# Optimization experiments

Hardware: AMD Instinct MI355X
Metric: run time of the kernel (lower is better)

## Reference

```python
import jax, jax.numpy as jnp
import numpy as np

N_NODES = 50000
N_EDGES = 800000
IN_FEATS, H_FEATS, N_CLASSES = 64, 64, 16


def setup_inputs() -> dict:
    key = jax.random.key(0)
    ks = jax.random.split(key, 8)
    x = jax.random.normal(ks[0], (N_NODES, IN_FEATS), dtype=jnp.float32)
    src = jax.random.randint(ks[1], (N_EDGES,), 0, N_NODES, dtype=jnp.int64)
    dst = jax.random.randint(ks[2], (N_EDGES,), 0, N_NODES, dtype=jnp.int64)
    W_self1 = jax.random.normal(ks[3], (IN_FEATS, H_FEATS), dtype=jnp.float32) / np.sqrt(IN_FEATS)
    W_neigh1 = jax.random.normal(ks[4], (IN_FEATS, H_FEATS), dtype=jnp.float32) / np.sqrt(IN_FEATS)
    b1 = jnp.zeros((H_FEATS,), dtype=jnp.float32)
    W_self2 = jax.random.normal(ks[5], (H_FEATS, N_CLASSES), dtype=jnp.float32) / np.sqrt(H_FEATS)
    W_neigh2 = jax.random.normal(ks[6], (H_FEATS, N_CLASSES), dtype=jnp.float32) / np.sqrt(H_FEATS)
    b2 = jnp.zeros((N_CLASSES,), dtype=jnp.float32)
    return {"x": x, "src": src, "dst": dst,
            "W_self1": W_self1, "W_neigh1": W_neigh1, "b1": b1,
            "W_self2": W_self2, "W_neigh2": W_neigh2, "b2": b2}


def _mean_agg(h, src, dst, n_nodes):
    # gather source-node features along edges, sum into destinations, divide by in-degree
    summed = jax.ops.segment_sum(h[src], dst, num_segments=n_nodes)  # [N, d]
    deg = jax.ops.segment_sum(jnp.ones_like(src, dtype=h.dtype), dst, num_segments=n_nodes)
    return summed / jnp.maximum(deg, 1.0)[:, None]  # zero in-degree -> zeros (DGL semantics)


def _sage_layer(h, src, dst, W_self, W_neigh, b):
    h_neigh = _mean_agg(h, src, dst, h.shape[0])
    return h @ W_self + h_neigh @ W_neigh + b


def reference(x, src, dst, W_self1, W_neigh1, b1, W_self2, W_neigh2, b2):
    h = _sage_layer(x, src, dst, W_self1, W_neigh1, b1)
    h = jax.nn.relu(h)
    out = _sage_layer(h, src, dst, W_self2, W_neigh2, b2)
    return out
```

## Files before the change

kernel.cpp:

```cpp
#include <hip/hip_runtime.h>
#include <hip/hip_bf16.h>
#include <cstring>


#define FEATS 64
#define CLS   16
#define EPT   16
#define CAP   5120
#define CAPN  64

typedef unsigned short bf16_t;
typedef float floatx2 __attribute__((ext_vector_type(2)));

__device__ __forceinline__ float bfbits2f(unsigned lo16) {
    unsigned v = lo16 << 16;
    float f;
    __builtin_memcpy(&f, &v, 4);
    return f;
}
__device__ __forceinline__ bf16_t f2bf(float f) {
    unsigned u;
    __builtin_memcpy(&u, &f, 4);
    u = (u + 0x7FFFu + ((u >> 16) & 1u)) >> 16;
    return (bf16_t)u;
}
__device__ __forceinline__ unsigned pack2(float a, float b) {
    return (unsigned)f2bf(a) | ((unsigned)f2bf(b) << 16);
}
__device__ __forceinline__ unsigned pack4_fp8(float a, float b, float c, float d) {
    int q = __builtin_amdgcn_cvt_pk_fp8_f32(a, b, 0, false);
    q = __builtin_amdgcn_cvt_pk_fp8_f32(c, d, q, true);
    return (unsigned)q;
}

__global__ __launch_bounds__(256) void fused_pg_kernel(
    const int* __restrict__ src, const int* __restrict__ dst,
    int* __restrict__ bucket_cnt, int* __restrict__ epart, int E,
    const float* __restrict__ x, const float* __restrict__ Ws,
    const float* __restrict__ Wn, bf16_t* __restrict__ selfo,
    unsigned char* __restrict__ t1, int N, int nbp)
{
    __shared__ float smem[16512];
    int t = threadIdx.x;

    if ((int)blockIdx.x < nbp) {
        int* hist = (int*)smem;
        int* base = hist + 256;
        int e0 = blockIdx.x * (256 * EPT);
        hist[t] = 0;
        __syncthreads();
        int pk[EPT];
        int bk[EPT];
#pragma unroll
        for (int j = 0; j < EPT; ++j) {
            int e = e0 + j * 256 + t;
            if (e < E) {
                int d = dst[e];
                pk[j] = (src[e] << 8) | (d & 255);
                bk[j] = d >> 8;
                atomicAdd(&hist[bk[j]], 1);
            } else bk[j] = -1;
        }
        __syncthreads();
        int c = hist[t];
        if (c) base[t] = atomicAdd(&bucket_cnt[t], c);
        hist[t] = 0;
        __syncthreads();
#pragma unroll
        for (int j = 0; j < EPT; ++j) {
            if (bk[j] >= 0) {
                int r = atomicAdd(&hist[bk[j]], 1);
                epart[bk[j] * CAP + base[bk[j]] + r] = pk[j];
            }
        }
        return;
    }

    float* Wc = smem;
    float* xs = smem + 8192;
    int node0 = ((int)blockIdx.x - nbp) * 128;

    for (int idx = t; idx < 64 * 128; idx += 256) {
        int k = idx >> 7, c = idx & 127;
        Wc[idx] = (c < 64) ? Ws[k * 64 + c] : Wn[k * 64 + (c - 64)];
    }
    for (int idx = t; idx < 128 * 16; idx += 256) {
        int row = idx >> 4, c4 = idx & 15;
        int node = node0 + row;
        float4 v = (node < N) ? ((const float4*)(x + (size_t)node * 64))[c4]
                              : make_float4(0.f, 0.f, 0.f, 0.f);
        float* p = &xs[row * 65 + c4 * 4];
        p[0] = v.x; p[1] = v.y; p[2] = v.z; p[3] = v.w;
    }
    __syncthreads();

    int m = t & 31;
    int g = t >> 5;
    float acc[4][16];
#pragma unroll
    for (int j = 0; j < 4; ++j)
#pragma unroll
        for (int c = 0; c < 16; ++c) acc[j][c] = 0.f;

    for (int k = 0; k < 64; ++k) {
        float w[16];
        const float* wp = &Wc[k * 128 + g * 16];
#pragma unroll
        for (int c = 0; c < 16; ++c) w[c] = wp[c];
        float a0 = xs[m * 65 + k];
        float a1 = xs[(m + 32) * 65 + k];
        float a2 = xs[(m + 64) * 65 + k];
        float a3 = xs[(m + 96) * 65 + k];
#pragma unroll
        for (int c = 0; c < 16; ++c) {
            acc[0][c] += a0 * w[c];
            acc[1][c] += a1 * w[c];
            acc[2][c] += a2 * w[c];
            acc[3][c] += a3 * w[c];
        }
    }
#pragma unroll
    for (int j = 0; j < 4; ++j) {
        int node = node0 + m + 32 * j;
        if (node < N) {
            if (g < 4) {
                bf16_t* dstp = selfo + (size_t)node * 64 + g * 16;
                uint4 p0, p1;
                p0.x = pack2(acc[j][0],  acc[j][1]);  p0.y = pack2(acc[j][2],  acc[j][3]);
                p0.z = pack2(acc[j][4],  acc[j][5]);  p0.w = pack2(acc[j][6],  acc[j][7]);
                p1.x = pack2(acc[j][8],  acc[j][9]);  p1.y = pack2(acc[j][10], acc[j][11]);
                p1.z = pack2(acc[j][12], acc[j][13]); p1.w = pack2(acc[j][14], acc[j][15]);
                *(uint4*)(dstp) = p0;
                *(uint4*)(dstp + 8) = p1;
            } else {
                unsigned char* dstp = t1 + (size_t)node * 64 + (g - 4) * 16;
                uint4 q;
                q.x = pack4_fp8(acc[j][0],  acc[j][1],  acc[j][2],  acc[j][3]);
                q.y = pack4_fp8(acc[j][4],  acc[j][5],  acc[j][6],  acc[j][7]);
                q.z = pack4_fp8(acc[j][8],  acc[j][9],  acc[j][10], acc[j][11]);
                q.w = pack4_fp8(acc[j][12], acc[j][13], acc[j][14], acc[j][15]);
                *(uint4*)(dstp) = q;
            }
        }
    }
}

__global__ __launch_bounds__(256) void buildcsr_kernel(const int* __restrict__ epart,
                                                       const int* __restrict__ bucket_cnt,
                                                       int* __restrict__ cnt,
                                                       int* __restrict__ csr, int N) {
    __shared__ int c[256];
    int t = threadIdx.x;
    int b = blockIdx.x;
    int ebeg = b * CAP;
    int ecnt = bucket_cnt[b];
    c[t] = 0;
    __syncthreads();
    for (int e = t; e < ecnt; e += 256) {
        int pk = epart[ebeg + e];
        int ln = pk & 255;
        int r = atomicAdd(&c[ln], 1);
        if (r < CAPN) csr[(size_t)(b * 256 + ln) * CAPN + r] = pk >> 8;
    }
    __syncthreads();
    int node = b * 256 + t;
    if (node < N) cnt[node] = c[t];
}

__global__ __launch_bounds__(256) void gather64_kernel(
    const int* __restrict__ csr, const int* __restrict__ cnt,
    const unsigned char* __restrict__ t1, const bf16_t* __restrict__ selfo,
    bf16_t* __restrict__ h1, const float* __restrict__ b1, int N)
{
    int wid = (blockIdx.x * 256 + threadIdx.x) >> 6;
    int lane = threadIdx.x & 63;
    int eslot = lane >> 4;
    int cg = lane & 15;
    if (wid >= N) return;
    int eraw = csr[(size_t)wid * CAPN + lane];
    int d = cnt[wid];
    size_t o = (size_t)wid * 64 + cg * 4;
    uint2 su;
    float4 bb;
    if (eslot == 0) {
        su = *(const uint2*)(selfo + o);
        bb = *(const float4*)(b1 + cg * 4);
    }
    d = min(d, CAPN);
    float ax = 0.f, ay = 0.f, az = 0.f, aw = 0.f;
    if (d > 0) {
        int dm1 = d - 1;
#define G64_ACC(r, m)                                                      \
        {                                                                  \
            floatx2 p_ = __builtin_amdgcn_cvt_pk_f32_fp8((int)(r), false); \
            floatx2 q_ = __builtin_amdgcn_cvt_pk_f32_fp8((int)(r), true);  \
            ax += (m) * p_.x; ay += (m) * p_.y;                            \
            az += (m) * q_.x; aw += (m) * q_.y;                            \
        }
#define G64_BATCH(KN)                                                      \
        {                                                                  \
            int ss[KN];                                                    \
            float mk[KN];                                                  \
            unsigned rr[KN];                                               \
            _Pragma("unroll")                                              \
            for (int k = 0; k < KN; ++k) {                                 \
                int i = eslot + 4 * k;                                     \
                int idx = i > dm1 ? dm1 : i;                               \
                mk[k] = (i <= dm1) ? 1.f : 0.f;                            \
                ss[k] = __shfl(eraw, idx);                                 \
            }                                                              \
            _Pragma("unroll")                                              \
            for (int k = 0; k < KN; ++k)                                   \
                rr[k] = *(const unsigned*)(t1 + (size_t)ss[k] * 64 + cg * 4); \
            _Pragma("unroll")                                              \
            for (int k = 0; k < KN; ++k) G64_ACC(rr[k], mk[k]);            \
        }
        if (d <= 16) {
            G64_BATCH(4)
        } else if (d <= 32) {
            G64_BATCH(8)
        } else {
            G64_BATCH(16)
        }
#undef G64_BATCH
#undef G64_ACC
        ax += __shfl_xor(ax, 16); ay += __shfl_xor(ay, 16);
        az += __shfl_xor(az, 16); aw += __shfl_xor(aw, 16);
        ax += __shfl_xor(ax, 32); ay += __shfl_xor(ay, 32);
        az += __shfl_xor(az, 32); aw += __shfl_xor(aw, 32);
    }
    if (eslot == 0) {
        float inv = 1.f / fmaxf((float)d, 1.f);
        float rx = fmaxf(bfbits2f(su.x & 0xffff) + ax * inv + bb.x, 0.f);
        float ry = fmaxf(bfbits2f(su.x >> 16)    + ay * inv + bb.y, 0.f);
        float rz = fmaxf(bfbits2f(su.y & 0xffff) + az * inv + bb.z, 0.f);
        float rw = fmaxf(bfbits2f(su.y >> 16)    + aw * inv + bb.w, 0.f);
        uint2 pk;
        pk.x = pack2(rx, ry);
        pk.y = pack2(rz, rw);
        *(uint2*)(h1 + o) = pk;
    }
}

__global__ __launch_bounds__(256) void gather16_kernel(
    const int* __restrict__ csr, const int* __restrict__ cnt,
    const bf16_t* __restrict__ t2,
    float* __restrict__ outp, const float* __restrict__ b2, int N)
{
    int wid = (blockIdx.x * 256 + threadIdx.x) >> 6;
    int lane = threadIdx.x & 63;
    int eslot = lane >> 3;
    int c2 = lane & 7;
    if (wid >= N) return;
    int eraw = csr[(size_t)wid * CAPN + lane];
    int d = cnt[wid];
    size_t o = (size_t)wid * 16 + c2 * 2;
    float2 oo = make_float2(0.f, 0.f), bbv = make_float2(0.f, 0.f);
    if (eslot == 0) {
        oo = *(const float2*)(outp + o);
        bbv = *(const float2*)(b2 + c2 * 2);
    }
    d = min(d, CAPN);
    float a0 = 0.f, a1 = 0.f;
    if (d > 0) {
        int dm1 = d - 1;
#define G16_BATCH(KN)                                                      \
        {                                                                  \
            int ss[KN];                                                    \
            float mk[KN];                                                  \
            unsigned uu[KN];                                               \
            _Pragma("unroll")                                              \
            for (int k = 0; k < KN; ++k) {                                 \
                int i = eslot + 8 * k;                                     \
                int idx = i > dm1 ? dm1 : i;                               \
                mk[k] = (i <= dm1) ? 1.f : 0.f;                            \
                ss[k] = __shfl(eraw, idx);                                 \
            }                                                              \
            _Pragma("unroll")                                              \
            for (int k = 0; k < KN; ++k)                                   \
                uu[k] = *(const unsigned*)(t2 + (size_t)ss[k] * 16 + c2 * 2); \
            _Pragma("unroll")                                              \
            for (int k = 0; k < KN; ++k) {                                 \
                a0 += mk[k] * bfbits2f(uu[k] & 0xffff);                    \
                a1 += mk[k] * bfbits2f(uu[k] >> 16);                       \
            }                                                              \
        }
        if (d <= 16) {
            G16_BATCH(2)
        } else if (d <= 32) {
            G16_BATCH(4)
        } else {
            G16_BATCH(8)
        }
#undef G16_BATCH
        a0 += __shfl_xor(a0, 8);  a1 += __shfl_xor(a1, 8);
        a0 += __shfl_xor(a0, 16); a1 += __shfl_xor(a1, 16);
        a0 += __shfl_xor(a0, 32); a1 += __shfl_xor(a1, 32);
    }
    if (eslot == 0) {
        float inv = 1.f / fmaxf((float)d, 1.f);
        float2 r;
        r.x = oo.x + a0 * inv + bbv.x;
        r.y = oo.y + a1 * inv + bbv.y;
        *(float2*)(outp + o) = r;
    }
}

__global__ __launch_bounds__(256) void gemm2_kernel(
    const bf16_t* __restrict__ h1, const float* __restrict__ Ws,
    const float* __restrict__ Wn, float* __restrict__ outp,
    bf16_t* __restrict__ t2, int N)
{
    __shared__ float Wc[64 * 32];
    __shared__ float xs[128 * 65];
    int t = threadIdx.x;
    int node0 = blockIdx.x * 128;

    for (int idx = t; idx < 64 * 32; idx += 256) {
        int k = idx >> 5, c = idx & 31;
        Wc[idx] = (c < 16) ? Ws[k * 16 + c] : Wn[k * 16 + (c - 16)];
    }
    for (int idx = t; idx < 128 * 8; idx += 256) {
        int row = idx >> 3, c8 = idx & 7;
        int node = node0 + row;
        float* p = &xs[row * 65 + c8 * 8];
        if (node < N) {
            uint4 u = *(const uint4*)(h1 + (size_t)node * 64 + c8 * 8);
            p[0] = bfbits2f(u.x & 0xffff); p[1] = bfbits2f(u.x >> 16);
            p[2] = bfbits2f(u.y & 0xffff); p[3] = bfbits2f(u.y >> 16);
            p[4] = bfbits2f(u.z & 0xffff); p[5] = bfbits2f(u.z >> 16);
            p[6] = bfbits2f(u.w & 0xffff); p[7] = bfbits2f(u.w >> 16);
        } else {
            for (int qq = 0; qq < 8; ++qq) p[qq] = 0.f;
        }
    }
    __syncthreads();

    int m = t & 31;
    int g = t >> 5;
    float acc[4][4];
#pragma unroll
    for (int j = 0; j < 4; ++j)
#pragma unroll
        for (int c = 0; c < 4; ++c) acc[j][c] = 0.f;

    for (int k = 0; k < 64; ++k) {
        float w[4];
        const float* wp = &Wc[k * 32 + g * 4];
#pragma unroll
        for (int c = 0; c < 4; ++c) w[c] = wp[c];
        float a0 = xs[m * 65 + k];
        float a1 = xs[(m + 32) * 65 + k];
        float a2 = xs[(m + 64) * 65 + k];
        float a3 = xs[(m + 96) * 65 + k];
#pragma unroll
        for (int c = 0; c < 4; ++c) {
            acc[0][c] += a0 * w[c];
            acc[1][c] += a1 * w[c];
            acc[2][c] += a2 * w[c];
            acc[3][c] += a3 * w[c];
        }
    }
#pragma unroll
    for (int j = 0; j < 4; ++j) {
        int node = node0 + m + 32 * j;
        if (node < N) {
            if (g < 4) {
                *(float4*)(outp + (size_t)node * 16 + g * 4) =
                    make_float4(acc[j][0], acc[j][1], acc[j][2], acc[j][3]);
            } else {
                uint2 pk;
                pk.x = pack2(acc[j][0], acc[j][1]);
                pk.y = pack2(acc[j][2], acc[j][3]);
                *(uint2*)(t2 + (size_t)node * 16 + (g - 4) * 4) = pk;
            }
        }
    }
}

extern "C" void kernel_launch(void* const* d_in, const int* in_sizes, int n_in,
                              void* d_out, int out_size, void* d_ws, size_t ws_size,
                              hipStream_t stream) {
    const float* x   = (const float*)d_in[0];
    const int*   src = (const int*)d_in[1];
    const int*   dst = (const int*)d_in[2];
    const float* Ws1 = (const float*)d_in[3];
    const float* Wn1 = (const float*)d_in[4];
    const float* b1  = (const float*)d_in[5];
    const float* Ws2 = (const float*)d_in[6];
    const float* Wn2 = (const float*)d_in[7];
    const float* b2  = (const float*)d_in[8];
    float* outp = (float*)d_out;

    const int N = in_sizes[0] / FEATS;
    const int E = in_sizes[1];
    const int B = (N + 255) / 256;
    const int NBP = (E + 256 * EPT - 1) / (256 * EPT);
    const int NBG = (N + 127) / 128;

    char* p = (char*)d_ws;
    auto align16 = [](char* q) { return (char*)(((size_t)q + 15) & ~(size_t)15); };
    int* bucket_cnt    = (int*)p;                  p = (char*)(bucket_cnt + 256);
    int* epart         = (int*)p;                  p = (char*)(epart + (size_t)B * CAP);
    int* cnt           = (int*)align16(p);         p = (char*)(cnt + N);
    int* csr           = (int*)align16(p);         p = (char*)(csr + (size_t)N * CAPN);
    bf16_t* selfo      = (bf16_t*)align16(p);      p = (char*)(selfo + (size_t)N * 64);
    unsigned char* t1  = (unsigned char*)align16(p); p = (char*)(t1 + (size_t)N * 64);
    bf16_t* h1         = (bf16_t*)align16(p);      p = (char*)(h1 + (size_t)N * 64);
    bf16_t* t2         = (bf16_t*)align16(p);

    hipMemsetAsync(bucket_cnt, 0, 256 * sizeof(int), stream);

    fused_pg_kernel<<<NBP + NBG, 256, 0, stream>>>(
        src, dst, bucket_cnt, epart, E, x, Ws1, Wn1, selfo, t1, N, NBP);
    buildcsr_kernel<<<B, 256, 0, stream>>>(epart, bucket_cnt, cnt, csr, N);

    gather64_kernel<<<((size_t)N * 64 + 255) / 256, 256, 0, stream>>>(
        csr, cnt, t1, selfo, h1, b1, N);
    gemm2_kernel<<<(N + 127) / 128, 256, 0, stream>>>(h1, Ws2, Wn2, outp, t2, N);
    gather16_kernel<<<((size_t)N * 64 + 255) / 256, 256, 0, stream>>>(
        csr, cnt, t2, outp, b2, N);
}
```

Before: 152.5 us.

## Merge all stages into one persistent cooperative kernel with grid syncs

Replaces the five separate launches (partition+GEMM1, CSR build, gather64, GEMM2, gather16) with one persistent cooperative kernel. The stages run as grid-stride loops separated by grid.sync(), which removes per-launch overhead and the idle gaps between kernels. GEMM tiles shrink from 128 to 64 nodes so the smaller shared-memory footprint allows three blocks per CU. In exchange, each stage is limited to a fixed grid, grid-wide barriers add cost, and register pressure under launch bounds of 3 may cause spills.

```diff
diff --git a/kernel.cpp b/kernel.cpp
--- a/kernel.cpp
+++ b/kernel.cpp
@@ -1,6 +1,9 @@
 #include <hip/hip_runtime.h>
+#include <hip/hip_cooperative_groups.h>
 #include <hip/hip_bf16.h>
 #include <cstring>
+
+namespace cgr = cooperative_groups;
 
 
 #define FEATS 64
@@ -8,6 +11,7 @@
 #define EPT   16
 #define CAP   5120
 #define CAPN  64
+#define SMEMF 12352
 
 typedef unsigned short bf16_t;
 typedef float floatx2 __attribute__((ext_vector_type(2)));
@@ -33,346 +37,330 @@
     return (unsigned)q;
 }
 
-__global__ __launch_bounds__(256) void fused_pg_kernel(
+__global__ __launch_bounds__(256, 3) void mega_kernel(
     const int* __restrict__ src, const int* __restrict__ dst,
-    int* __restrict__ bucket_cnt, int* __restrict__ epart, int E,
-    const float* __restrict__ x, const float* __restrict__ Ws,
-    const float* __restrict__ Wn, bf16_t* __restrict__ selfo,
-    unsigned char* __restrict__ t1, int N, int nbp)
+    int* __restrict__ bucket_cnt, int* __restrict__ epart,
+    int* __restrict__ cnt, int* __restrict__ csr,
+    const float* __restrict__ x,
+    const float* __restrict__ Ws1, const float* __restrict__ Wn1,
+    const float* __restrict__ b1,
+    const float* __restrict__ Ws2, const float* __restrict__ Wn2,
+    const float* __restrict__ b2,
+    bf16_t* __restrict__ selfo, unsigned char* __restrict__ t1,
+    bf16_t* __restrict__ h1, bf16_t* __restrict__ t2,
+    float* __restrict__ outp, int N, int E)
 {
-    __shared__ float smem[16512];
-    int t = threadIdx.x;
-
-    if ((int)blockIdx.x < nbp) {
-        int* hist = (int*)smem;
-        int* base = hist + 256;
-        int e0 = blockIdx.x * (256 * EPT);
-        hist[t] = 0;
+    __shared__ float smem[SMEMF];
+    cgr::grid_group grid = cgr::this_grid();
+    const int t = threadIdx.x;
+    const int nb = gridDim.x;
+    const int NP = (E + 256 * EPT - 1) / (256 * EPT);
+    const int NT = (N + 63) / 64;
+    const int B  = (N + 255) / 256;
+
+    for (int u = (int)blockIdx.x; u < NP + NT; u += nb) {
+        if (u < NP) {
+            int* hist = (int*)smem;
+            int* base = hist + 256;
+            int e0 = u * (256 * EPT);
+            hist[t] = 0;
+            __syncthreads();
+            int pk[EPT], bk[EPT];
+#pragma unroll
+            for (int j = 0; j < EPT; ++j) {
+                int e = e0 + j * 256 + t;
+                if (e < E) {
+                    int d = dst[e];
+                    pk[j] = (src[e] << 8) | (d & 255);
+                    bk[j] = d >> 8;
+                    atomicAdd(&hist[bk[j]], 1);
+                } else bk[j] = -1;
+            }
+            __syncthreads();
+            int c0 = hist[t];
+            if (c0) base[t] = atomicAdd(&bucket_cnt[t], c0);
+            hist[t] = 0;
+            __syncthreads();
+#pragma unroll
+            for (int j = 0; j < EPT; ++j) {
+                if (bk[j] >= 0) {
+                    int r = atomicAdd(&hist[bk[j]], 1);
+                    epart[bk[j] * CAP + base[bk[j]] + r] = pk[j];
+                }
+            }
+            __syncthreads();
+        } else {
+            int node0 = (u - NP) * 64;
+            float* Wc = smem;
+            float* xs = smem + 8192;
+            for (int idx = t; idx < 64 * 128; idx += 256) {
+                int k = idx >> 7, c = idx & 127;
+                Wc[idx] = (c < 64) ? Ws1[k * 64 + c] : Wn1[k * 64 + (c - 64)];
+            }
+            for (int idx = t; idx < 64 * 16; idx += 256) {
+                int row = idx >> 4, c4 = idx & 15;
+                int node = node0 + row;
+                float4 v = (node < N) ? ((const float4*)(x + (size_t)node * 64))[c4]
+                                      : make_float4(0.f, 0.f, 0.f, 0.f);
+                float* pp = &xs[row * 65 + c4 * 4];
+                pp[0] = v.x; pp[1] = v.y; pp[2] = v.z; pp[3] = v.w;
+            }
+            __syncthreads();
+            int m = t & 31;
+            int g = t >> 5;
+            float acc[2][16];
+#pragma unroll
+            for (int j = 0; j < 2; ++j)
+#pragma unroll
+                for (int c = 0; c < 16; ++c) acc[j][c] = 0.f;
+            for (int k = 0; k < 64; ++k) {
+                float w[16];
+                const float* wp = &Wc[k * 128 + g * 16];
+#pragma unroll
+                for (int c = 0; c < 16; ++c) w[c] = wp[c];
+                float a0 = xs[m * 65 + k];
+                float a1 = xs[(m + 32) * 65 + k];
+#pragma unroll
+                for (int c = 0; c < 16; ++c) {
+                    acc[0][c] += a0 * w[c];
+                    acc[1][c] += a1 * w[c];
+                }
+            }
+#pragma unroll
+            for (int j = 0; j < 2; ++j) {
+                int node = node0 + m + 32 * j;
+                if (node < N) {
+                    if (g < 4) {
+                        bf16_t* dstp = selfo + (size_t)node * 64 + g * 16;
+                        uint4 p0, p1;
+                        p0.x = pack2(acc[j][0],  acc[j][1]);  p0.y = pack2(acc[j][2],  acc[j][3]);
+                        p0.z = pack2(acc[j][4],  acc[j][5]);  p0.w = pack2(acc[j][6],  acc[j][7]);
+                        p1.x = pack2(acc[j][8],  acc[j][9]);  p1.y = pack2(acc[j][10], acc[j][11]);
+                        p1.z = pack2(acc[j][12], acc[j][13]); p1.w = pack2(acc[j][14], acc[j][15]);
+                        *(uint4*)(dstp) = p0;
+                        *(uint4*)(dstp + 8) = p1;
+                    } else {
+                        unsigned char* dstp = t1 + (size_t)node * 64 + (g - 4) * 16;
+                        uint4 q;
+                        q.x = pack4_fp8(acc[j][0],  acc[j][1],  acc[j][2],  acc[j][3]);
+                        q.y = pack4_fp8(acc[j][4],  acc[j][5],  acc[j][6],  acc[j][7]);
+                        q.z = pack4_fp8(acc[j][8],  acc[j][9],  acc[j][10], acc[j][11]);
+                        q.w = pack4_fp8(acc[j][12], acc[j][13], acc[j][14], acc[j][15]);
+                        *(uint4*)(dstp) = q;
+                    }
+                }
+            }
+            __syncthreads();
+        }
+    }
+    grid.sync();
+
+    for (int u = (int)blockIdx.x; u < B; u += nb) {
+        int* c = (int*)smem;
+        int ebeg = u * CAP;
+        int ecnt = bucket_cnt[u];
+        c[t] = 0;
         __syncthreads();
-        int pk[EPT];
-        int bk[EPT];
-#pragma unroll
-        for (int j = 0; j < EPT; ++j) {
-            int e = e0 + j * 256 + t;
-            if (e < E) {
-                int d = dst[e];
-                pk[j] = (src[e] << 8) | (d & 255);
-                bk[j] = d >> 8;
-                atomicAdd(&hist[bk[j]], 1);
-            } else bk[j] = -1;
+        for (int e = t; e < ecnt; e += 256) {
+            int pk = epart[ebeg + e];
+            int ln = pk & 255;
+            int r = atomicAdd(&c[ln], 1);
+            if (r < CAPN) csr[(size_t)(u * 256 + ln) * CAPN + r] = pk >> 8;
         }
         __syncthreads();
-        int c = hist[t];
-        if (c) base[t] = atomicAdd(&bucket_cnt[t], c);
-        hist[t] = 0;
+        int node = u * 256 + t;
+        if (node < N) cnt[node] = c[t];
         __syncthreads();
-#pragma unroll
-        for (int j = 0; j < EPT; ++j) {
-            if (bk[j] >= 0) {
-                int r = atomicAdd(&hist[bk[j]], 1);
-                epart[bk[j] * CAP + base[bk[j]] + r] = pk[j];
-            }
-        }
-        return;
-    }
-
-    float* Wc = smem;
-    float* xs = smem + 8192;
-    int node0 = ((int)blockIdx.x - nbp) * 128;
-
-    for (int idx = t; idx < 64 * 128; idx += 256) {
-        int k = idx >> 7, c = idx & 127;
-        Wc[idx] = (c < 64) ? Ws[k * 64 + c] : Wn[k * 64 + (c - 64)];
-    }
-    for (int idx = t; idx < 128 * 16; idx += 256) {
-        int row = idx >> 4, c4 = idx & 15;
-        int node = node0 + row;
-        float4 v = (node < N) ? ((const float4*)(x + (size_t)node * 64))[c4]
-                              : make_float4(0.f, 0.f, 0.f, 0.f);
-        float* p = &xs[row * 65 + c4 * 4];
-        p[0] = v.x; p[1] = v.y; p[2] = v.z; p[3] = v.w;
-    }
-    __syncthreads();
-
-    int m = t & 31;
-    int g = t >> 5;
-    float acc[4][16];
-#pragma unroll
-    for (int j = 0; j < 4; ++j)
-#pragma unroll
-        for (int c = 0; c < 16; ++c) acc[j][c] = 0.f;
-
-    for (int k = 0; k < 64; ++k) {
-        float w[16];
-        const float* wp = &Wc[k * 128 + g * 16];
-#pragma unroll
-        for (int c = 0; c < 16; ++c) w[c] = wp[c];
-        float a0 = xs[m * 65 + k];
-        float a1 = xs[(m + 32) * 65 + k];
-        float a2 = xs[(m + 64) * 65 + k];
-        float a3 = xs[(m + 96) * 65 + k];
-#pragma unroll
-        for (int c = 0; c < 16; ++c) {
-            acc[0][c] += a0 * w[c];
-            acc[1][c] += a1 * w[c];
-            acc[2][c] += a2 * w[c];
-            acc[3][c] += a3 * w[c];
-        }
-    }
-#pragma unroll
-    for (int j = 0; j < 4; ++j) {
-        int node = node0 + m + 32 * j;
-        if (node < N) {
-            if (g < 4) {
-                bf16_t* dstp = selfo + (size_t)node * 64 + g * 16;
-                uint4 p0, p1;
-                p0.x = pack2(acc[j][0],  acc[j][1]);  p0.y = pack2(acc[j][2],  acc[j][3]);
-                p0.z = pack2(acc[j][4],  acc[j][5]);  p0.w = pack2(acc[j][6],  acc[j][7]);
-                p1.x = pack2(acc[j][8],  acc[j][9]);  p1.y = pack2(acc[j][10], acc[j][11]);
-                p1.z = pack2(acc[j][12], acc[j][13]); p1.w = pack2(acc[j][14], acc[j][15]);
-                *(uint4*)(dstp) = p0;
-                *(uint4*)(dstp + 8) = p1;
-            } else {
-                unsigned char* dstp = t1 + (size_t)node * 64 + (g - 4) * 16;
-                uint4 q;
-                q.x = pack4_fp8(acc[j][0],  acc[j][1],  acc[j][2],  acc[j][3]);
-                q.y = pack4_fp8(acc[j][4],  acc[j][5],  acc[j][6],  acc[j][7]);
-                q.z = pack4_fp8(acc[j][8],  acc[j][9],  acc[j][10], acc[j][11]);
-                q.w = pack4_fp8(acc[j][12], acc[j][13], acc[j][14], acc[j][15]);
-                *(uint4*)(dstp) = q;
-            }
-        }
-    }
-}
-
-__global__ __launch_bounds__(256) void buildcsr_kernel(const int* __restrict__ epart,
-                                                       const int* __restrict__ bucket_cnt,
-                                                       int* __restrict__ cnt,
-                                                       int* __restrict__ csr, int N) {
-    __shared__ int c[256];
-    int t = threadIdx.x;
-    int b = blockIdx.x;
-    int ebeg = b * CAP;
-    int ecnt = bucket_cnt[b];
-    c[t] = 0;
-    __syncthreads();
-    for (int e = t; e < ecnt; e += 256) {
-        int pk = epart[ebeg + e];
-        int ln = pk & 255;
-        int r = atomicAdd(&c[ln], 1);
-        if (r < CAPN) csr[(size_t)(b * 256 + ln) * CAPN + r] = pk >> 8;
-    }
-    __syncthreads();
-    int node = b * 256 + t;
-    if (node < N) cnt[node] = c[t];
-}
-
-__global__ __launch_bounds__(256) void gather64_kernel(
-    const int* __restrict__ csr, const int* __restrict__ cnt,
-    const unsigned char* __restrict__ t1, const bf16_t* __restrict__ selfo,
-    bf16_t* __restrict__ h1, const float* __restrict__ b1, int N)
-{
-    int wid = (blockIdx.x * 256 + threadIdx.x) >> 6;
-    int lane = threadIdx.x & 63;
-    int eslot = lane >> 4;
-    int cg = lane & 15;
-    if (wid >= N) return;
-    int eraw = csr[(size_t)wid * CAPN + lane];
-    int d = cnt[wid];
-    size_t o = (size_t)wid * 64 + cg * 4;
-    uint2 su;
-    float4 bb;
-    if (eslot == 0) {
-        su = *(const uint2*)(selfo + o);
-        bb = *(const float4*)(b1 + cg * 4);
-    }
-    d = min(d, CAPN);
-    float ax = 0.f, ay = 0.f, az = 0.f, aw = 0.f;
-    if (d > 0) {
-        int dm1 = d - 1;
+    }
+    grid.sync();
+
+    {
+        const int lane = t & 63;
+        const int eslot = lane >> 4;
+        const int cg4 = lane & 15;
+        const int gw = (int)blockIdx.x * 4 + (t >> 6);
+        for (int wid = gw; wid < N; wid += nb * 4) {
+            int eraw = csr[(size_t)wid * CAPN + lane];
+            int d = cnt[wid];
+            size_t o = (size_t)wid * 64 + cg4 * 4;
+            uint2 su; float4 bb;
+            if (eslot == 0) {
+                su = *(const uint2*)(selfo + o);
+                bb = *(const float4*)(b1 + cg4 * 4);
+            }
+            d = min(d, CAPN);
+            float ax = 0.f, ay = 0.f, az = 0.f, aw = 0.f;
+            if (d > 0) {
+                int dm1 = d - 1;
 #define G64_ACC(r, m)                                                      \
-        {                                                                  \
-            floatx2 p_ = __builtin_amdgcn_cvt_pk_f32_fp8((int)(r), false); \
-            floatx2 q_ = __builtin_amdgcn_cvt_pk_f32_fp8((int)(r), true);  \
-            ax += (m) * p_.x; ay += (m) * p_.y;                            \
-            az += (m) * q_.x; aw += (m) * q_.y;                            \
-        }
+                {                                                          \
+                    floatx2 p_ = __builtin_amdgcn_cvt_pk_f32_fp8((int)(r), false); \
+                    floatx2 q_ = __builtin_amdgcn_cvt_pk_f32_fp8((int)(r), true);  \
+                    ax += (m) * p_.x; ay += (m) * p_.y;                    \
+                    az += (m) * q_.x; aw += (m) * q_.y;                    \
+                }
 #define G64_BATCH(KN)                                                      \
-        {                                                                  \
-            int ss[KN];                                                    \
-            float mk[KN];                                                  \
-            unsigned rr[KN];                                               \
-            _Pragma("unroll")                                              \
-            for (int k = 0; k < KN; ++k) {                                 \
-                int i = eslot + 4 * k;                                     \
-                int idx = i > dm1 ? dm1 : i;                               \
-                mk[k] = (i <= dm1) ? 1.f : 0.f;                            \
-                ss[k] = __shfl(eraw, idx);                                 \
-            }                                                              \
-            _Pragma("unroll")                                              \
-            for (int k = 0; k < KN; ++k)                                   \
-                rr[k] = *(const unsigned*)(t1 + (size_t)ss[k] * 64 + cg * 4); \
-            _Pragma("unroll")                                              \
-            for (int k = 0; k < KN; ++k) G64_ACC(rr[k], mk[k]);            \
-        }
-        if (d <= 16) {
-            G64_BATCH(4)
-        } else if (d <= 32) {
-            G64_BATCH(8)
-        } else {
-            G64_BATCH(16)
-        }
+                {                                                          \
+                    int ss[KN]; float mk[KN]; unsigned rr[KN];             \
+                    _Pragma("unroll")                                      \
+                    for (int k = 0; k < KN; ++k) {                         \
+                        int i = eslot + 4 * k;                             \
+                        int idx = i > dm1 ? dm1 : i;                       \
+                        mk[k] = (i <= dm1) ? 1.f : 0.f;                    \
+                        ss[k] = __shfl(eraw, idx);                         \
+                    }                                                      \
+                    _Pragma("unroll")                                      \
+                    for (int k = 0; k < KN; ++k)                           \
+                        rr[k] = *(const unsigned*)(t1 + (size_t)ss[k] * 64 + cg4 * 4); \
+                    _Pragma("unroll")                                      \
+                    for (int k = 0; k < KN; ++k) G64_ACC(rr[k], mk[k]);    \
+                }
+                if (d <= 16) {
+                    G64_BATCH(4)
+                } else if (d <= 32) {
+                    G64_BATCH(8)
+                } else {
+                    G64_BATCH(16)
+                }
 #undef G64_BATCH
 #undef G64_ACC
-        ax += __shfl_xor(ax, 16); ay += __shfl_xor(ay, 16);
-        az += __shfl_xor(az, 16); aw += __shfl_xor(aw, 16);
-        ax += __shfl_xor(ax, 32); ay += __shfl_xor(ay, 32);
-        az += __shfl_xor(az, 32); aw += __shfl_xor(aw, 32);
-    }
-    if (eslot == 0) {
-        float inv = 1.f / fmaxf((float)d, 1.f);
-        float rx = fmaxf(bfbits2f(su.x & 0xffff) + ax * inv + bb.x, 0.f);
-        float ry = fmaxf(bfbits2f(su.x >> 16)    + ay * inv + bb.y, 0.f);
-        float rz = fmaxf(bfbits2f(su.y & 0xffff) + az * inv + bb.z, 0.f);
-        float rw = fmaxf(bfbits2f(su.y >> 16)    + aw * inv + bb.w, 0.f);
-        uint2 pk;
-        pk.x = pack2(rx, ry);
-        pk.y = pack2(rz, rw);
-        *(uint2*)(h1 + o) = pk;
-    }
-}
-
-__global__ __launch_bounds__(256) void gather16_kernel(
-    const int* __restrict__ csr, const int* __restrict__ cnt,
-    const bf16_t* __restrict__ t2,
-    float* __restrict__ outp, const float* __restrict__ b2, int N)
-{
-    int wid = (blockIdx.x * 256 + threadIdx.x) >> 6;
-    int lane = threadIdx.x & 63;
-    int eslot = lane >> 3;
-    int c2 = lane & 7;
-    if (wid >= N) return;
-    int eraw = csr[(size_t)wid * CAPN + lane];
-    int d = cnt[wid];
-    size_t o = (size_t)wid * 16 + c2 * 2;
-    float2 oo = make_float2(0.f, 0.f), bbv = make_float2(0.f, 0.f);
-    if (eslot == 0) {
-        oo = *(const float2*)(outp + o);
-        bbv = *(const float2*)(b2 + c2 * 2);
-    }
-    d = min(d, CAPN);
-    float a0 = 0.f, a1 = 0.f;
-    if (d > 0) {
-        int dm1 = d - 1;
+                ax += __shfl_xor(ax, 16); ay += __shfl_xor(ay, 16);
+                az += __shfl_xor(az, 16); aw += __shfl_xor(aw, 16);
+                ax += __shfl_xor(ax, 32); ay += __shfl_xor(ay, 32);
+                az += __shfl_xor(az, 32); aw += __shfl_xor(aw, 32);
+            }
+            if (eslot == 0) {
+                float inv = 1.f / fmaxf((float)d, 1.f);
+                float rx = fmaxf(bfbits2f(su.x & 0xffff) + ax * inv + bb.x, 0.f);
+                float ry = fmaxf(bfbits2f(su.x >> 16)    + ay * inv + bb.y, 0.f);
+                float rz = fmaxf(bfbits2f(su.y & 0xffff) + az * inv + bb.z, 0.f);
+                float rw = fmaxf(bfbits2f(su.y >> 16)    + aw * inv + bb.w, 0.f);
+                uint2 pk;
+                pk.x = pack2(rx, ry);
+                pk.y = pack2(rz, rw);
+                *(uint2*)(h1 + o) = pk;
+            }
+        }
+    }
+    grid.sync();
+
+    for (int u = (int)blockIdx.x; u < NT; u += nb) {
+        int node0 = u * 64;
+        float* Wc2 = smem;
+        float* xs2 = smem + 2048;
+        for (int idx = t; idx < 64 * 32; idx += 256) {
+            int k = idx >> 5, c = idx & 31;
+            Wc2[idx] = (c < 16) ? Ws2[k * 16 + c] : Wn2[k * 16 + (c - 16)];
+        }
+        for (int idx = t; idx < 64 * 8; idx += 256) {
+            int row = idx >> 3, c8 = idx & 7;
+            int node = node0 + row;
+            float* pp = &xs2[row * 65 + c8 * 8];
+            if (node < N) {
+                uint4 uv = *(const uint4*)(h1 + (size_t)node * 64 + c8 * 8);
+                pp[0] = bfbits2f(uv.x & 0xffff); pp[1] = bfbits2f(uv.x >> 16);
+                pp[2] = bfbits2f(uv.y & 0xffff); pp[3] = bfbits2f(uv.y >> 16);
+                pp[4] = bfbits2f(uv.z & 0xffff); pp[5] = bfbits2f(uv.z >> 16);
+                pp[6] = bfbits2f(uv.w & 0xffff); pp[7] = bfbits2f(uv.w >> 16);
+            } else {
+                for (int qq = 0; qq < 8; ++qq) pp[qq] = 0.f;
+            }
+        }
+        __syncthreads();
+        int m = t & 31;
+        int g = t >> 5;
+        float acc[2][4];
+#pragma unroll
+        for (int j = 0; j < 2; ++j)
+#pragma unroll
+            for (int c = 0; c < 4; ++c) acc[j][c] = 0.f;
+        for (int k = 0; k < 64; ++k) {
+            float w[4];
+            const float* wp = &Wc2[k * 32 + g * 4];
+#pragma unroll
+            for (int c = 0; c < 4; ++c) w[c] = wp[c];
+            float a0 = xs2[m * 65 + k];
+            float a1 = xs2[(m + 32) * 65 + k];
+#pragma unroll
+            for (int c = 0; c < 4; ++c) {
+                acc[0][c] += a0 * w[c];
+                acc[1][c] += a1 * w[c];
+            }
+        }
+#pragma unroll
+        for (int j = 0; j < 2; ++j) {
+            int node = node0 + m + 32 * j;
+            if (node < N) {
+                if (g < 4) {
+                    *(float4*)(outp + (size_t)node * 16 + g * 4) =
+                        make_float4(acc[j][0], acc[j][1], acc[j][2], acc[j][3]);
+                } else {
+                    uint2 pk;
+                    pk.x = pack2(acc[j][0], acc[j][1]);
+                    pk.y = pack2(acc[j][2], acc[j][3]);
+                    *(uint2*)(t2 + (size_t)node * 16 + (g - 4) * 4) = pk;
+                }
+            }
+        }
+        __syncthreads();
+    }
+    grid.sync();
+
+    {
+        const int lane = t & 63;
+        const int eslot = lane >> 3;
+        const int c2 = lane & 7;
+        const int gw = (int)blockIdx.x * 4 + (t >> 6);
+        for (int wid = gw; wid < N; wid += nb * 4) {
+            int eraw = csr[(size_t)wid * CAPN + lane];
+            int d = cnt[wid];
+            size_t o = (size_t)wid * 16 + c2 * 2;
+            float2 oo = make_float2(0.f, 0.f), bbv = make_float2(0.f, 0.f);
+            if (eslot == 0) {
+                oo = *(const float2*)(outp + o);
+                bbv = *(const float2*)(b2 + c2 * 2);
+            }
+            d = min(d, CAPN);
+            float a0 = 0.f, a1 = 0.f;
+            if (d > 0) {
+                int dm1 = d - 1;
 #define G16_BATCH(KN)                                                      \
-        {                                                                  \
-            int ss[KN];                                                    \
-            float mk[KN];                                                  \
-            unsigned uu[KN];                                               \
-            _Pragma("unroll")                                              \
-            for (int k = 0; k < KN; ++k) {                                 \
-                int i = eslot + 8 * k;                                     \
-                int idx = i > dm1 ? dm1 : i;                               \
-                mk[k] = (i <= dm1) ? 1.f : 0.f;                            \
-                ss[k] = __shfl(eraw, idx);                                 \
-            }                                                              \
-            _Pragma("unroll")                                              \
-            for (int k = 0; k < KN; ++k)                                   \
-                uu[k] = *(const unsigned*)(t2 + (size_t)ss[k] * 16 + c2 * 2); \
-            _Pragma("unroll")                                              \
-            for (int k = 0; k < KN; ++k) {                                 \
-                a0 += mk[k] * bfbits2f(uu[k] & 0xffff);                    \
-                a1 += mk[k] * bfbits2f(uu[k] >> 16);                       \
-            }                                                              \
-        }
-        if (d <= 16) {
-            G16_BATCH(2)
-        } else if (d <= 32) {
-            G16_BATCH(4)
-        } else {
-            G16_BATCH(8)
-        }
+                {                                                          \
+                    int ss[KN]; float mk[KN]; unsigned uu[KN];             \
+                    _Pragma("unroll")                                      \
+                    for (int k = 0; k < KN; ++k) {                         \
+                        int i = eslot + 8 * k;                             \
+                        int idx = i > dm1 ? dm1 : i;                       \
+                        mk[k] = (i <= dm1) ? 1.f : 0.f;                    \
+                        ss[k] = __shfl(eraw, idx);                         \
+                    }                                                      \
+                    _Pragma("unroll")                                      \
+                    for (int k = 0; k < KN; ++k)                           \
+                        uu[k] = *(const unsigned*)(t2 + (size_t)ss[k] * 16 + c2 * 2); \
+                    _Pragma("unroll")                                      \
+                    for (int k = 0; k < KN; ++k) {                         \
+                        a0 += mk[k] * bfbits2f(uu[k] & 0xffff);            \
+                        a1 += mk[k] * bfbits2f(uu[k] >> 16);               \
+                    }                                                      \
+                }
+                if (d <= 16) {
+                    G16_BATCH(2)
+                } else if (d <= 32) {
+                    G16_BATCH(4)
+                } else {
+                    G16_BATCH(8)
+                }
 #undef G16_BATCH
-        a0 += __shfl_xor(a0, 8);  a1 += __shfl_xor(a1, 8);
-        a0 += __shfl_xor(a0, 16); a1 += __shfl_xor(a1, 16);
-        a0 += __shfl_xor(a0, 32); a1 += __shfl_xor(a1, 32);
-    }
-    if (eslot == 0) {
-        float inv = 1.f / fmaxf((float)d, 1.f);
-        float2 r;
-        r.x = oo.x + a0 * inv + bbv.x;
-        r.y = oo.y + a1 * inv + bbv.y;
-        *(float2*)(outp + o) = r;
-    }
-}
-
-__global__ __launch_bounds__(256) void gemm2_kernel(
-    const bf16_t* __restrict__ h1, const float* __restrict__ Ws,
-    const float* __restrict__ Wn, float* __restrict__ outp,
-    bf16_t* __restrict__ t2, int N)
-{
-    __shared__ float Wc[64 * 32];
-    __shared__ float xs[128 * 65];
-    int t = threadIdx.x;
-    int node0 = blockIdx.x * 128;
-
-    for (int idx = t; idx < 64 * 32; idx += 256) {
-        int k = idx >> 5, c = idx & 31;
-        Wc[idx] = (c < 16) ? Ws[k * 16 + c] : Wn[k * 16 + (c - 16)];
-    }
-    for (int idx = t; idx < 128 * 8; idx += 256) {
-        int row = idx >> 3, c8 = idx & 7;
-        int node = node0 + row;
-        float* p = &xs[row * 65 + c8 * 8];
-        if (node < N) {
-            uint4 u = *(const uint4*)(h1 + (size_t)node * 64 + c8 * 8);
-            p[0] = bfbits2f(u.x & 0xffff); p[1] = bfbits2f(u.x >> 16);
-            p[2] = bfbits2f(u.y & 0xffff); p[3] = bfbits2f(u.y >> 16);
-            p[4] = bfbits2f(u.z & 0xffff); p[5] = bfbits2f(u.z >> 16);
-            p[6] = bfbits2f(u.w & 0xffff); p[7] = bfbits2f(u.w >> 16);
-        } else {
-            for (int qq = 0; qq < 8; ++qq) p[qq] = 0.f;
-        }
-    }
-    __syncthreads();
-
-    int m = t & 31;
-    int g = t >> 5;
-    float acc[4][4];
-#pragma unroll
-    for (int j = 0; j < 4; ++j)
-#pragma unroll
-        for (int c = 0; c < 4; ++c) acc[j][c] = 0.f;
-
-    for (int k = 0; k < 64; ++k) {
-        float w[4];
-        const float* wp = &Wc[k * 32 + g * 4];
-#pragma unroll
-        for (int c = 0; c < 4; ++c) w[c] = wp[c];
-        float a0 = xs[m * 65 + k];
-        float a1 = xs[(m + 32) * 65 + k];
-        float a2 = xs[(m + 64) * 65 + k];
-        float a3 = xs[(m + 96) * 65 + k];
-#pragma unroll
-        for (int c = 0; c < 4; ++c) {
-            acc[0][c] += a0 * w[c];
-            acc[1][c] += a1 * w[c];
-            acc[2][c] += a2 * w[c];
-            acc[3][c] += a3 * w[c];
-        }
-    }
-#pragma unroll
-    for (int j = 0; j < 4; ++j) {
-        int node = node0 + m + 32 * j;
-        if (node < N) {
-            if (g < 4) {
-                *(float4*)(outp + (size_t)node * 16 + g * 4) =
-                    make_float4(acc[j][0], acc[j][1], acc[j][2], acc[j][3]);
-            } else {
-                uint2 pk;
-                pk.x = pack2(acc[j][0], acc[j][1]);
-                pk.y = pack2(acc[j][2], acc[j][3]);
-                *(uint2*)(t2 + (size_t)node * 16 + (g - 4) * 4) = pk;
+                a0 += __shfl_xor(a0, 8);  a1 += __shfl_xor(a1, 8);
+                a0 += __shfl_xor(a0, 16); a1 += __shfl_xor(a1, 16);
+                a0 += __shfl_xor(a0, 32); a1 += __shfl_xor(a1, 32);
+            }
+            if (eslot == 0) {
+                float inv = 1.f / fmaxf((float)d, 1.f);
+                float2 r;
+                r.x = oo.x + a0 * inv + bbv.x;
+                r.y = oo.y + a1 * inv + bbv.y;
+                *(float2*)(outp + o) = r;
             }
         }
     }
@@ -381,9 +369,9 @@
 extern "C" void kernel_launch(void* const* d_in, const int* in_sizes, int n_in,
                               void* d_out, int out_size, void* d_ws, size_t ws_size,
                               hipStream_t stream) {
+    const int* srcp = (const int*)d_in[1];
+    const int* dstp = (const int*)d_in[2];
     const float* x   = (const float*)d_in[0];
-    const int*   src = (const int*)d_in[1];
-    const int*   dst = (const int*)d_in[2];
     const float* Ws1 = (const float*)d_in[3];
     const float* Wn1 = (const float*)d_in[4];
     const float* b1  = (const float*)d_in[5];
@@ -392,11 +380,9 @@
     const float* b2  = (const float*)d_in[8];
     float* outp = (float*)d_out;
 
-    const int N = in_sizes[0] / FEATS;
-    const int E = in_sizes[1];
+    int N = in_sizes[0] / FEATS;
+    int E = in_sizes[1];
     const int B = (N + 255) / 256;
-    const int NBP = (E + 256 * EPT - 1) / (256 * EPT);
-    const int NBG = (N + 127) / 128;
 
     char* p = (char*)d_ws;
     auto align16 = [](char* q) { return (char*)(((size_t)q + 15) & ~(size_t)15); };
@@ -409,15 +395,29 @@
     bf16_t* h1         = (bf16_t*)align16(p);      p = (char*)(h1 + (size_t)N * 64);
     bf16_t* t2         = (bf16_t*)align16(p);
 
+    static int grid_blocks = 0;
+    if (grid_blocks == 0) {
+        int bpc = 0;
+        if (hipOccupancyMaxActiveBlocksPerMultiprocessor(&bpc, mega_kernel, 256, 0)
+                != hipSuccess || bpc <= 0)
+            bpc = 2;
+        int ncu = 256;
+        hipDeviceProp_t prop;
+        if (hipGetDeviceProperties(&prop, 0) == hipSuccess && prop.multiProcessorCount > 0)
+            ncu = prop.multiProcessorCount;
+        grid_blocks = bpc * ncu;
+    }
+
     hipMemsetAsync(bucket_cnt, 0, 256 * sizeof(int), stream);
 
-    fused_pg_kernel<<<NBP + NBG, 256, 0, stream>>>(
-        src, dst, bucket_cnt, epart, E, x, Ws1, Wn1, selfo, t1, N, NBP);
-    buildcsr_kernel<<<B, 256, 0, stream>>>(epart, bucket_cnt, cnt, csr, N);
-
-    gather64_kernel<<<((size_t)N * 64 + 255) / 256, 256, 0, stream>>>(
-        csr, cnt, t1, selfo, h1, b1, N);
-    gemm2_kernel<<<(N + 127) / 128, 256, 0, stream>>>(h1, Ws2, Wn2, outp, t2, N);
-    gather16_kernel<<<((size_t)N * 64 + 255) / 256, 256, 0, stream>>>(
-        csr, cnt, t2, outp, b2, N);
-}
+    void* kargs[] = {
+        (void*)&srcp, (void*)&dstp, (void*)&bucket_cnt, (void*)&epart,
+        (void*)&cnt, (void*)&csr, (void*)&x,
+        (void*)&Ws1, (void*)&Wn1, (void*)&b1,
+        (void*)&Ws2, (void*)&Wn2, (void*)&b2,
+        (void*)&selfo, (void*)&t1, (void*)&h1, (void*)&t2,
+        (void*)&outp, (void*)&N, (void*)&E
+    };
+    hipLaunchCooperativeKernel((void*)mega_kernel, dim3(grid_blocks), dim3(256),
+                               kargs, 0, stream);
+}
```

New measurement: 483.7 us. 217% more time.

## Fuse layer-1 neighbor gather with layer-2 GEMM via shared memory

Applied to the files above, without the earlier changes.

Merges the 64-wide gather kernel and the second-layer GEMM into one kernel. Each block of 256 threads gathers 64 nodes (16 rows per wave) into a shared fp32 tile, then runs the 64x32 projection to produce the self output and t2. This removes the h1 bf16 round trip through global memory and one kernel launch. In exchange, each block now processes its gather rows sequentially and uses more shared memory, which could lower occupancy and latency hiding for the irregular gather loads.

```diff
diff --git a/kernel.cpp b/kernel.cpp
--- a/kernel.cpp
+++ b/kernel.cpp
@@ -167,78 +167,129 @@
     if (node < N) cnt[node] = c[t];
 }
 
-__global__ __launch_bounds__(256) void gather64_kernel(
+__global__ __launch_bounds__(256) void fused_g64g2_kernel(
     const int* __restrict__ csr, const int* __restrict__ cnt,
     const unsigned char* __restrict__ t1, const bf16_t* __restrict__ selfo,
-    bf16_t* __restrict__ h1, const float* __restrict__ b1, int N)
+    const float* __restrict__ b1,
+    const float* __restrict__ Ws2, const float* __restrict__ Wn2,
+    float* __restrict__ outp, bf16_t* __restrict__ t2, int N)
 {
-    int wid = (blockIdx.x * 256 + threadIdx.x) >> 6;
-    int lane = threadIdx.x & 63;
+    __shared__ float Wc[64 * 32];
+    __shared__ float xs[64 * 65];
+    int t = threadIdx.x;
+    int node0 = blockIdx.x * 64;
+
+    for (int idx = t; idx < 64 * 32; idx += 256) {
+        int k = idx >> 5, c = idx & 31;
+        Wc[idx] = (c < 16) ? Ws2[k * 16 + c] : Wn2[k * 16 + (c - 16)];
+    }
+
+    int wv = t >> 6;
+    int lane = t & 63;
     int eslot = lane >> 4;
-    int cg = lane & 15;
-    if (wid >= N) return;
-    int eraw = csr[(size_t)wid * CAPN + lane];
-    int d = cnt[wid];
-    size_t o = (size_t)wid * 64 + cg * 4;
-    uint2 su;
-    float4 bb;
-    if (eslot == 0) {
-        su = *(const uint2*)(selfo + o);
-        bb = *(const float4*)(b1 + cg * 4);
-    }
-    d = min(d, CAPN);
-    float ax = 0.f, ay = 0.f, az = 0.f, aw = 0.f;
-    if (d > 0) {
-        int dm1 = d - 1;
+    int cg4 = lane & 15;
+    float4 bb = *(const float4*)(b1 + cg4 * 4);
+
+    for (int it = 0; it < 16; ++it) {
+        int row = it * 4 + wv;
+        int wid = node0 + row;
+        if (wid < N) {
+            int eraw = csr[(size_t)wid * CAPN + lane];
+            int d = cnt[wid];
+            size_t o = (size_t)wid * 64 + cg4 * 4;
+            uint2 su;
+            if (eslot == 0) su = *(const uint2*)(selfo + o);
+            d = min(d, CAPN);
+            float ax = 0.f, ay = 0.f, az = 0.f, aw = 0.f;
+            if (d > 0) {
+                int dm1 = d - 1;
 #define G64_ACC(r, m)                                                      \
-        {                                                                  \
-            floatx2 p_ = __builtin_amdgcn_cvt_pk_f32_fp8((int)(r), false); \
-            floatx2 q_ = __builtin_amdgcn_cvt_pk_f32_fp8((int)(r), true);  \
-            ax += (m) * p_.x; ay += (m) * p_.y;                            \
-            az += (m) * q_.x; aw += (m) * q_.y;                            \
-        }
+                {                                                          \
+                    floatx2 p_ = __builtin_amdgcn_cvt_pk_f32_fp8((int)(r), false); \
+                    floatx2 q_ = __builtin_amdgcn_cvt_pk_f32_fp8((int)(r), true);  \
+                    ax += (m) * p_.x; ay += (m) * p_.y;                    \
+                    az += (m) * q_.x; aw += (m) * q_.y;                    \
+                }
 #define G64_BATCH(KN)                                                      \
-        {                                                                  \
-            int ss[KN];                                                    \
-            float mk[KN];                                                  \
-            unsigned rr[KN];                                               \
-            _Pragma("unroll")                                              \
-            for (int k = 0; k < KN; ++k) {                                 \
-                int i = eslot + 4 * k;                                     \
-                int idx = i > dm1 ? dm1 : i;                               \
-                mk[k] = (i <= dm1) ? 1.f : 0.f;                            \
-                ss[k] = __shfl(eraw, idx);                                 \
-            }                                                              \
-            _Pragma("unroll")                                              \
-            for (int k = 0; k < KN; ++k)                                   \
-                rr[k] = *(const unsigned*)(t1 + (size_t)ss[k] * 64 + cg * 4); \
-            _Pragma("unroll")                                              \
-            for (int k = 0; k < KN; ++k) G64_ACC(rr[k], mk[k]);            \
-        }
-        if (d <= 16) {
-            G64_BATCH(4)
-        } else if (d <= 32) {
-            G64_BATCH(8)
-        } else {
-            G64_BATCH(16)
-        }
+                {                                                          \
+                    int ss[KN]; float mk[KN]; unsigned rr[KN];             \
+                    _Pragma("unroll")                                      \
+                    for (int k = 0; k < KN; ++k) {                         \
+                        int i = eslot + 4 * k;                             \
+                        int idx = i > dm1 ? dm1 : i;                       \
+                        mk[k] = (i <= dm1) ? 1.f : 0.f;                    \
+                        ss[k] = __shfl(eraw, idx);                         \
+                    }                                                      \
+                    _Pragma("unroll")                                      \
+                    for (int k = 0; k < KN; ++k)                           \
+                        rr[k] = *(const unsigned*)(t1 + (size_t)ss[k] * 64 + cg4 * 4); \
+                    _Pragma("unroll")                                      \
+                    for (int k = 0; k < KN; ++k) G64_ACC(rr[k], mk[k]);    \
+                }
+                if (d <= 16) {
+                    G64_BATCH(4)
+                } else if (d <= 32) {
+                    G64_BATCH(8)
+                } else {
+                    G64_BATCH(16)
+                }
 #undef G64_BATCH
 #undef G64_ACC
-        ax += __shfl_xor(ax, 16); ay += __shfl_xor(ay, 16);
-        az += __shfl_xor(az, 16); aw += __shfl_xor(aw, 16);
-        ax += __shfl_xor(ax, 32); ay += __shfl_xor(ay, 32);
-        az += __shfl_xor(az, 32); aw += __shfl_xor(aw, 32);
-    }
-    if (eslot == 0) {
-        float inv = 1.f / fmaxf((float)d, 1.f);
-        float rx = fmaxf(bfbits2f(su.x & 0xffff) + ax * inv + bb.x, 0.f);
-        float ry = fmaxf(bfbits2f(su.x >> 16)    + ay * inv + bb.y, 0.f);
-        float rz = fmaxf(bfbits2f(su.y & 0xffff) + az * inv + bb.z, 0.f);
-        float rw = fmaxf(bfbits2f(su.y >> 16)    + aw * inv + bb.w, 0.f);
-        uint2 pk;
-        pk.x = pack2(rx, ry);
-        pk.y = pack2(rz, rw);
-        *(uint2*)(h1 + o) = pk;
+                ax += __shfl_xor(ax, 16); ay += __shfl_xor(ay, 16);
+                az += __shfl_xor(az, 16); aw += __shfl_xor(aw, 16);
+                ax += __shfl_xor(ax, 32); ay += __shfl_xor(ay, 32);
+                az += __shfl_xor(az, 32); aw += __shfl_xor(aw, 32);
+            }
+            if (eslot == 0) {
+                float inv = 1.f / fmaxf((float)d, 1.f);
+                float* pp = &xs[row * 65 + cg4 * 4];
+                pp[0] = fmaxf(bfbits2f(su.x & 0xffff) + ax * inv + bb.x, 0.f);
+                pp[1] = fmaxf(bfbits2f(su.x >> 16)    + ay * inv + bb.y, 0.f);
+                pp[2] = fmaxf(bfbits2f(su.y & 0xffff) + az * inv + bb.z, 0.f);
+                pp[3] = fmaxf(bfbits2f(su.y >> 16)    + aw * inv + bb.w, 0.f);
+            }
+        } else if (eslot == 0) {
+            float* pp = &xs[row * 65 + cg4 * 4];
+            pp[0] = 0.f; pp[1] = 0.f; pp[2] = 0.f; pp[3] = 0.f;
+        }
+    }
+    __syncthreads();
+
+    int m = t & 31;
+    int g = t >> 5;
+    float acc[2][4];
+#pragma unroll
+    for (int j = 0; j < 2; ++j)
+#pragma unroll
+        for (int c = 0; c < 4; ++c) acc[j][c] = 0.f;
+
+    for (int k = 0; k < 64; ++k) {
+        float w[4];
+        const float* wp = &Wc[k * 32 + g * 4];
+#pragma unroll
+        for (int c = 0; c < 4; ++c) w[c] = wp[c];
+        float a0 = xs[m * 65 + k];
+        float a1 = xs[(m + 32) * 65 + k];
+#pragma unroll
+        for (int c = 0; c < 4; ++c) {
+            acc[0][c] += a0 * w[c];
+            acc[1][c] += a1 * w[c];
+        }
+    }
+#pragma unroll
+    for (int j = 0; j < 2; ++j) {
+        int node = node0 + m + 32 * j;
+        if (node < N) {
+            if (g < 4) {
+                *(float4*)(outp + (size_t)node * 16 + g * 4) =
+                    make_float4(acc[j][0], acc[j][1], acc[j][2], acc[j][3]);
+            } else {
+                uint2 pk;
+                pk.x = pack2(acc[j][0], acc[j][1]);
+                pk.y = pack2(acc[j][2], acc[j][3]);
+                *(uint2*)(t2 + (size_t)node * 16 + (g - 4) * 4) = pk;
+            }
+        }
     }
 }
 
@@ -266,9 +317,7 @@
         int dm1 = d - 1;
 #define G16_BATCH(KN)                                                      \
         {                                                                  \
-            int ss[KN];                                                    \
-            float mk[KN];                                                  \
-            unsigned uu[KN];                                               \
+            int ss[KN]; float mk[KN]; unsigned uu[KN];                     \
             _Pragma("unroll")                                              \
             for (int k = 0; k < KN; ++k) {                                 \
                 int i = eslot + 8 * k;                                     \
@@ -306,78 +355,6 @@
     }
 }
 
-__global__ __launch_bounds__(256) void gemm2_kernel(
-    const bf16_t* __restrict__ h1, const float* __restrict__ Ws,
-    const float* __restrict__ Wn, float* __restrict__ outp,
-    bf16_t* __restrict__ t2, int N)
-{
-    __shared__ float Wc[64 * 32];
-    __shared__ float xs[128 * 65];
-    int t = threadIdx.x;
-    int node0 = blockIdx.x * 128;
-
-    for (int idx = t; idx < 64 * 32; idx += 256) {
-        int k = idx >> 5, c = idx & 31;
-        Wc[idx] = (c < 16) ? Ws[k * 16 + c] : Wn[k * 16 + (c - 16)];
-    }
-    for (int idx = t; idx < 128 * 8; idx += 256) {
-        int row = idx >> 3, c8 = idx & 7;
-        int node = node0 + row;
-        float* p = &xs[row * 65 + c8 * 8];
-        if (node < N) {
-            uint4 u = *(const uint4*)(h1 + (size_t)node * 64 + c8 * 8);
-            p[0] = bfbits2f(u.x & 0xffff); p[1] = bfbits2f(u.x >> 16);
-            p[2] = bfbits2f(u.y & 0xffff); p[3] = bfbits2f(u.y >> 16);
-            p[4] = bfbits2f(u.z & 0xffff); p[5] = bfbits2f(u.z >> 16);
-            p[6] = bfbits2f(u.w & 0xffff); p[7] = bfbits2f(u.w >> 16);
-        } else {
-            for (int qq = 0; qq < 8; ++qq) p[qq] = 0.f;
-        }
-    }
-    __syncthreads();
-
-    int m = t & 31;
-    int g = t >> 5;
-    float acc[4][4];
-#pragma unroll
-    for (int j = 0; j < 4; ++j)
-#pragma unroll
-        for (int c = 0; c < 4; ++c) acc[j][c] = 0.f;
-
-    for (int k = 0; k < 64; ++k) {
-        float w[4];
-        const float* wp = &Wc[k * 32 + g * 4];
-#pragma unroll
-        for (int c = 0; c < 4; ++c) w[c] = wp[c];
-        float a0 = xs[m * 65 + k];
-        float a1 = xs[(m + 32) * 65 + k];
-        float a2 = xs[(m + 64) * 65 + k];
-        float a3 = xs[(m + 96) * 65 + k];
-#pragma unroll
-        for (int c = 0; c < 4; ++c) {
-            acc[0][c] += a0 * w[c];
-            acc[1][c] += a1 * w[c];
-            acc[2][c] += a2 * w[c];
-            acc[3][c] += a3 * w[c];
-        }
-    }
-#pragma unroll
-    for (int j = 0; j < 4; ++j) {
-        int node = node0 + m + 32 * j;
-        if (node < N) {
-            if (g < 4) {
-                *(float4*)(outp + (size_t)node * 16 + g * 4) =
-                    make_float4(acc[j][0], acc[j][1], acc[j][2], acc[j][3]);
-            } else {
-                uint2 pk;
-                pk.x = pack2(acc[j][0], acc[j][1]);
-                pk.y = pack2(acc[j][2], acc[j][3]);
-                *(uint2*)(t2 + (size_t)node * 16 + (g - 4) * 4) = pk;
-            }
-        }
-    }
-}
-
 extern "C" void kernel_launch(void* const* d_in, const int* in_sizes, int n_in,
                               void* d_out, int out_size, void* d_ws, size_t ws_size,
                               hipStream_t stream) {
@@ -397,6 +374,7 @@
     const int B = (N + 255) / 256;
     const int NBP = (E + 256 * EPT - 1) / (256 * EPT);
     const int NBG = (N + 127) / 128;
+    const int NG2 = (N + 63) / 64;
 
     char* p = (char*)d_ws;
     auto align16 = [](char* q) { return (char*)(((size_t)q + 15) & ~(size_t)15); };
@@ -406,7 +384,6 @@
     int* csr           = (int*)align16(p);         p = (char*)(csr + (size_t)N * CAPN);
     bf16_t* selfo      = (bf16_t*)align16(p);      p = (char*)(selfo + (size_t)N * 64);
     unsigned char* t1  = (unsigned char*)align16(p); p = (char*)(t1 + (size_t)N * 64);
-    bf16_t* h1         = (bf16_t*)align16(p);      p = (char*)(h1 + (size_t)N * 64);
     bf16_t* t2         = (bf16_t*)align16(p);
 
     hipMemsetAsync(bucket_cnt, 0, 256 * sizeof(int), stream);
@@ -415,9 +392,8 @@
         src, dst, bucket_cnt, epart, E, x, Ws1, Wn1, selfo, t1, N, NBP);
     buildcsr_kernel<<<B, 256, 0, stream>>>(epart, bucket_cnt, cnt, csr, N);
 
-    gather64_kernel<<<((size_t)N * 64 + 255) / 256, 256, 0, stream>>>(
-        csr, cnt, t1, selfo, h1, b1, N);
-    gemm2_kernel<<<(N + 127) / 128, 256, 0, stream>>>(h1, Ws2, Wn2, outp, t2, N);
+    fused_g64g2_kernel<<<NG2, 256, 0, stream>>>(
+        csr, cnt, t1, selfo, b1, Ws2, Wn2, outp, t2, N);
     gather16_kernel<<<((size_t)N * 64 + 255) / 256, 256, 0, stream>>>(
         csr, cnt, t2, outp, b2, N);
 }
```

Result: slower. 220.7 us (+44.7%).
